# Kernel tuning notes

Measured on AMD Instinct MI355X. Metric: run time of the kernel, lower is better.

## Reference

```python
import jax, jax.numpy as jnp
import numpy as np

CAPACITY_RATIO = 0.75  # matches init kwarg


def setup_inputs() -> dict:
    key = jax.random.key(0)
    k1, k2, k3 = jax.random.split(key, 3)
    B, L, D = 4, 8192, 1024
    x = jax.random.normal(k1, (B, L, D), dtype=jnp.float32)
    # router: nn.Linear(dim, 1, bias=False) -> weight vector [D]
    w_router = jax.random.normal(k2, (D,), dtype=jnp.float32) * 0.02
    # block_fn instantiated as GELU(Linear(D, D)) applied to selected tokens
    w_block = jax.random.normal(k3, (D, D), dtype=jnp.float32) * 0.02
    return {"x": x, "w_router": w_router, "w_block": w_block}


def reference(x, w_router, w_block):
    # Inference path of MoDRouter.forward (self.training == False)
    B, L, D = x.shape
    k = max(1, int(L * CAPACITY_RATIO))  # 6144 < L, so routing path taken
    # scores = self.router(x).squeeze(-1)  -> [B, L]
    scores = jnp.einsum('bld,d->bl', x, w_router)
    # top-k token selection per batch row
    _, top_idx = jax.lax.top_k(scores, k)  # [B, k]
    # gather selected tokens: [B, k, D]
    selected = jnp.take_along_axis(x, top_idx[:, :, None], axis=1)
    # block_fn(selected, None): GELU(selected @ w_block)
    processed = jax.nn.gelu(jnp.einsum('bkd,de->bke', selected, w_block))
    # scatter processed tokens back; unselected tokens pass through (residual skip)
    batch_idx = jnp.arange(B)[:, None]  # [B, 1]
    out = x.at[batch_idx, top_idx].set(processed)
    return out
```

## Files before the change

### kernel.cpp

```cpp
#include <hip/hip_runtime.h>
#include <hip/hip_bf16.h>

typedef unsigned short u16;
typedef unsigned int u32;
typedef __attribute__((ext_vector_type(8))) short short8;
typedef __attribute__((ext_vector_type(4))) float f32x4;

#define L_TOK 8192
#define BATCH 4
#define DIM 1024
#define KSEL 6144
#define NTOK (BATCH * L_TOK)

__device__ __forceinline__ u16 f2bf(float f) {
    u32 u = __float_as_uint(f);
    return (u16)((u + 0x7fffu + ((u >> 16) & 1u)) >> 16);
}
__device__ __forceinline__ u32 cvt2(float a, float b) {
    __hip_bfloat162 h = __float22bfloat162_rn(float2{a, b});
    u32 r;
    __builtin_memcpy(&r, &h, 4);
    return r;
}
__device__ __forceinline__ float gelu_tanh(float v) {
    float inner = 0.7978845608028654f * (v + 0.044715f * v * v * v);
    return 0.5f * v * (1.0f + tanhf(inner));
}
__device__ __forceinline__ void async_copy16(const void* g, void* l) {
    __builtin_amdgcn_global_load_lds(
        (const __attribute__((address_space(1))) void*)g,
        (__attribute__((address_space(3))) void*)l, 16, 0, 0);
}

__global__ __launch_bounds__(256) void score_kernel(const float* __restrict__ x,
                                                    const float* __restrict__ wr,
                                                    float* __restrict__ scores) {
    int token = blockIdx.x * 4 + (threadIdx.x >> 6);
    int lane = threadIdx.x & 63;
    const float4* xr = (const float4*)(x + (size_t)token * DIM) + lane * 4;
    const float4* wp = (const float4*)wr + lane * 4;
    double acc = 0.0;
#pragma unroll
    for (int c = 0; c < 4; ++c) {
        float4 xv = xr[c];
        float4 wv = wp[c];
        acc += (double)xv.x * wv.x + (double)xv.y * wv.y +
               (double)xv.z * wv.z + (double)xv.w * wv.w;
    }
#pragma unroll
    for (int off = 32; off > 0; off >>= 1) acc += __shfl_down(acc, off, 64);
    if (lane == 0) scores[token] = (float)acc;
}

__global__ __launch_bounds__(1024) void select_kernel(const float* __restrict__ scores,
                                                      int* __restrict__ mask) {
    __shared__ u32 keys[L_TOK];
    __shared__ int hist[256];
    __shared__ int g0[256], g1[256];
    __shared__ int wsum[16];
    __shared__ int sel_digit, greater_cnt;
    const int b = blockIdx.x;
    const int tid = threadIdx.x;
    const int lane = tid & 63, wid = tid >> 6;
    const float* s = scores + (size_t)b * L_TOK;
    for (int i = tid; i < L_TOK; i += 1024) {
        u32 u = __float_as_uint(s[i]);
        keys[i] = (u & 0x80000000u) ? ~u : (u | 0x80000000u);
    }

    u32 prefix = 0;
    int need = KSEL;
#pragma unroll
    for (int pass = 0; pass < 4; ++pass) {
        const int shift = 24 - 8 * pass;
        const u32 pmask = (pass == 0) ? 0u : (0xFFFFFFFFu << (shift + 8));
        if (tid < 256) hist[tid] = 0;
        __syncthreads();
        for (int i = tid; i < L_TOK; i += 1024) {
            u32 key = keys[i];
            if ((key & pmask) == prefix)
                atomicAdd(&hist[(key >> shift) & 0xffu], 1);
        }
        __syncthreads();
        if (tid < 256) g0[tid] = hist[tid];
        __syncthreads();
        int* src = g0;
        int* dst = g1;
        for (int step = 1; step < 256; step <<= 1) {
            if (tid < 256) {
                int v = src[tid];
                if (tid + step < 256) v += src[tid + step];
                dst[tid] = v;
            }
            __syncthreads();
            int* t = src; src = dst; dst = t;
        }
        if (tid < 256) {
            int Gd = src[tid];
            int Gn = (tid == 255) ? 0 : src[tid + 1];
            if (Gd >= need && Gn < need) { sel_digit = tid; greater_cnt = Gn; }
        }
        __syncthreads();
        prefix |= ((u32)sel_digit) << shift;
        need -= greater_cnt;
        __syncthreads();
    }
    const u32 T = prefix;
    const int need_eq = need;

    const int base = tid * 8;
    u32 kv[8];
    int eq = 0;
#pragma unroll
    for (int c = 0; c < 8; ++c) { kv[c] = keys[base + c]; eq += (kv[c] == T); }
    int inc = eq;
#pragma unroll
    for (int off = 1; off < 64; off <<= 1) {
        int n = __shfl_up(inc, off, 64);
        if (lane >= off) inc += n;
    }
    if (lane == 63) wsum[wid] = inc;
    __syncthreads();
    int wbase = 0;
    for (int w = 0; w < wid; ++w) wbase += wsum[w];
    int rank = wbase + inc - eq;
    int sel[8];
#pragma unroll
    for (int c = 0; c < 8; ++c) {
        u32 key = kv[c];
        int se = 0;
        if (key > T) se = 1;
        else if (key == T) { se = (rank < need_eq) ? 1 : 0; rank++; }
        sel[c] = se;
    }
    int4* mp = (int4*)(mask + (size_t)b * L_TOK + base);
    mp[0] = int4{sel[0], sel[1], sel[2], sel[3]};
    mp[1] = int4{sel[4], sel[5], sel[6], sel[7]};
}

__global__ __launch_bounds__(256) void transpose_kernel(const float* __restrict__ W,
                                                        u16* __restrict__ WT) {
    __shared__ u16 tile[32][33];
    int bx = blockIdx.x * 32, by = blockIdx.y * 32;
    int tx = threadIdx.x & 31, ty = threadIdx.x >> 5;
    for (int r = ty; r < 32; r += 8)
        tile[r][tx] = f2bf(W[(size_t)(by + r) * DIM + bx + tx]);
    __syncthreads();
    for (int r = ty; r < 32; r += 8)
        WT[(size_t)(bx + r) * DIM + by + tx] = tile[tx][r];
}

__global__ __launch_bounds__(256) void cvt_kernel(const float* __restrict__ x,
                                                  u16* __restrict__ xb) {
    size_t i = ((size_t)blockIdx.x * 256 + threadIdx.x) * 8;
    float4 v0 = *(const float4*)(x + i);
    float4 v1 = *(const float4*)(x + i + 4);
    union { short8 s; u32 u[4]; } pk;
    pk.u[0] = cvt2(v0.x, v0.y); pk.u[1] = cvt2(v0.z, v0.w);
    pk.u[2] = cvt2(v1.x, v1.y); pk.u[3] = cvt2(v1.z, v1.w);
    *(short8*)(xb + i) = pk.s;
}

#define BM 128
#define BN 128
#define BK 32

__global__ __launch_bounds__(256) void gemm_bf16_kernel(const u16* __restrict__ Xb,
                                                        const u16* __restrict__ WT,
                                                        const int* __restrict__ mask,
                                                        float* __restrict__ out) {
    __shared__ alignas(16) u16 As[BM * BK];
    __shared__ alignas(16) u16 Bs[BN * BK];
    const int tid = threadIdx.x;
    const int wave = tid >> 6, lane = tid & 63;
    const int wm = wave >> 1, wn = wave & 1;
    const size_t rowbase = (size_t)blockIdx.x * BM;
    const int colbase = blockIdx.y * BN;

    f32x4 acc[4][4] = {};

    const int ca0 = tid, ca1 = tid + 256;
    const int r0 = ca0 >> 2, k0 = (ca0 & 3) * 8;
    const int r1 = ca1 >> 2, k1 = (ca1 & 3) * 8;
    const int q = lane >> 4, mrow = lane & 15;

    for (int kt = 0; kt < DIM; kt += BK) {
        async_copy16(Xb + (rowbase + r0) * DIM + kt + k0, As + ca0 * 8);
        async_copy16(Xb + (rowbase + r1) * DIM + kt + k1, As + ca1 * 8);
        async_copy16(WT + (size_t)(colbase + r0) * DIM + kt + k0, Bs + ca0 * 8);
        async_copy16(WT + (size_t)(colbase + r1) * DIM + kt + k1, Bs + ca1 * 8);
        __syncthreads();

        short8 a[4], b[4];
#pragma unroll
        for (int i = 0; i < 4; ++i)
            a[i] = *(const short8*)(As + (wm * 64 + i * 16 + mrow) * BK + q * 8);
#pragma unroll
        for (int j = 0; j < 4; ++j)
            b[j] = *(const short8*)(Bs + (wn * 64 + j * 16 + mrow) * BK + q * 8);
#pragma unroll
        for (int i = 0; i < 4; ++i)
#pragma unroll
            for (int j = 0; j < 4; ++j)
                acc[i][j] = __builtin_amdgcn_mfma_f32_16x16x32_bf16(a[i], b[j], acc[i][j], 0, 0, 0);
        __syncthreads();
    }

#pragma unroll
    for (int i = 0; i < 4; ++i) {
#pragma unroll
        for (int r = 0; r < 4; ++r) {
            size_t grow = rowbase + wm * 64 + i * 16 + q * 4 + r;
            if (mask[grow]) {
#pragma unroll
                for (int j = 0; j < 4; ++j) {
                    float g = gelu_tanh(acc[i][j][r]);
                    int col = colbase + wn * 64 + j * 16 + mrow;
                    out[grow * DIM + col] = g;
                }
            }
        }
    }
}

__global__ __launch_bounds__(256) void gemm_f32_kernel(const float* __restrict__ X,
                                                       const u16* __restrict__ WT,
                                                       const int* __restrict__ mask,
                                                       float* __restrict__ out) {
    __shared__ alignas(16) u16 As[BM * BK];
    __shared__ alignas(16) u16 Bs[BN * BK];
    const int tid = threadIdx.x;
    const int wave = tid >> 6, lane = tid & 63;
    const int wm = wave >> 1, wn = wave & 1;
    const size_t rowbase = (size_t)blockIdx.x * BM;
    const int colbase = blockIdx.y * BN;

    f32x4 acc[4][4] = {};

    const int cb0 = tid, cb1 = tid + 256;
    const int br0 = cb0 >> 2, bk0 = (cb0 & 3) * 8;
    const int br1 = cb1 >> 2, bk1 = (cb1 & 3) * 8;
    const int arow = tid >> 1, ahalf = tid & 1;
    const int q = lane >> 4, mrow = lane & 15;

    for (int kt = 0; kt < DIM; kt += BK) {
        async_copy16(WT + (size_t)(colbase + br0) * DIM + kt + bk0, Bs + cb0 * 8);
        async_copy16(WT + (size_t)(colbase + br1) * DIM + kt + bk1, Bs + cb1 * 8);

        const float4* xp = (const float4*)(X + (rowbase + arow) * DIM + kt + ahalf * 16);
        float4 v0 = xp[0], v1 = xp[1], v2 = xp[2], v3 = xp[3];
        union { short8 s[2]; u32 u[8]; } pk;
        pk.u[0] = cvt2(v0.x, v0.y); pk.u[1] = cvt2(v0.z, v0.w);
        pk.u[2] = cvt2(v1.x, v1.y); pk.u[3] = cvt2(v1.z, v1.w);
        pk.u[4] = cvt2(v2.x, v2.y); pk.u[5] = cvt2(v2.z, v2.w);
        pk.u[6] = cvt2(v3.x, v3.y); pk.u[7] = cvt2(v3.z, v3.w);
        *(short8*)(As + arow * BK + ahalf * 16)     = pk.s[0];
        *(short8*)(As + arow * BK + ahalf * 16 + 8) = pk.s[1];

        __syncthreads();

        short8 a[4], b[4];
#pragma unroll
        for (int i = 0; i < 4; ++i)
            a[i] = *(const short8*)(As + (wm * 64 + i * 16 + mrow) * BK + q * 8);
#pragma unroll
        for (int j = 0; j < 4; ++j)
            b[j] = *(const short8*)(Bs + (wn * 64 + j * 16 + mrow) * BK + q * 8);
#pragma unroll
        for (int i = 0; i < 4; ++i)
#pragma unroll
            for (int j = 0; j < 4; ++j)
                acc[i][j] = __builtin_amdgcn_mfma_f32_16x16x32_bf16(a[i], b[j], acc[i][j], 0, 0, 0);
        __syncthreads();
    }

#pragma unroll
    for (int i = 0; i < 4; ++i) {
#pragma unroll
        for (int r = 0; r < 4; ++r) {
            size_t grow = rowbase + wm * 64 + i * 16 + q * 4 + r;
            if (mask[grow]) {
#pragma unroll
                for (int j = 0; j < 4; ++j) {
                    float g = gelu_tanh(acc[i][j][r]);
                    int col = colbase + wn * 64 + j * 16 + mrow;
                    out[grow * DIM + col] = g;
                }
            }
        }
    }
}

__global__ __launch_bounds__(256) void passthrough_kernel(const float* __restrict__ x,
                                                          const int* __restrict__ mask,
                                                          float* __restrict__ out) {
    size_t c = (size_t)blockIdx.x * 256 + threadIdx.x;
    int token = (int)(c >> 8);
    if (!mask[token]) {
        ((float4*)out)[c] = ((const float4*)x)[c];
    }
}

extern "C" void kernel_launch(void* const* d_in, const int* in_sizes, int n_in,
                              void* d_out, int out_size, void* d_ws, size_t ws_size,
                              hipStream_t stream) {
    const float* x  = (const float*)d_in[0];
    const float* wr = (const float*)d_in[1];
    const float* wb = (const float*)d_in[2];
    float* out = (float*)d_out;

    float* scores = (float*)d_ws;
    int*   mask   = (int*)((char*)d_ws + NTOK * 4);
    u16*   WT     = (u16*)((char*)d_ws + NTOK * 8);
    u16*   Xb     = (u16*)((char*)d_ws + NTOK * 8 + DIM * DIM * 2);

    const size_t need_ws = (size_t)NTOK * 8 + (size_t)DIM * DIM * 2
                         + (size_t)NTOK * DIM * 2;

    score_kernel<<<NTOK / 4, 256, 0, stream>>>(x, wr, scores);
    select_kernel<<<BATCH, 1024, 0, stream>>>(scores, mask);
    transpose_kernel<<<dim3(DIM / 32, DIM / 32), 256, 0, stream>>>(wb, WT);
    if (ws_size >= need_ws) {
        cvt_kernel<<<(NTOK * (DIM / 8)) / 256, 256, 0, stream>>>(x, Xb);
        gemm_bf16_kernel<<<dim3(NTOK / BM, DIM / BN), 256, 0, stream>>>(Xb, WT, mask, out);
    } else {
        gemm_f32_kernel<<<dim3(NTOK / BM, DIM / BN), 256, 0, stream>>>(x, WT, mask, out);
    }
    passthrough_kernel<<<(NTOK * 256) / 256, 256, 0, stream>>>(x, mask, out);
}
```

Measured before the change: 381.6 us.

## Compact selected tokens, fuse bf16 cast into scoring, and swizzle GEMM LDS

The select kernel now also emits compacted index lists of selected and unselected tokens. The GEMM runs only over the selected rows, gathered through those indices, instead of computing all tokens and masking the output. The bf16 conversion of x is folded into the score kernel, which removes one full read pass over x. The GEMM uses a BK of 64 with an XOR-swizzled LDS layout to cut bank conflicts. GELU switches from tanh to a sigmoid form using __expf, and the passthrough copy works per unselected token. The costs are gathered row loads and a slightly different GELU approximation.

```diff
diff --git a/kernel.cpp b/kernel.cpp
--- a/kernel.cpp
+++ b/kernel.cpp
@@ -11,6 +11,8 @@
 #define DIM 1024
 #define KSEL 6144
 #define NTOK (BATCH * L_TOK)
+#define NSEL (BATCH * KSEL)
+#define NUNSEL (NTOK - NSEL)
 
 __device__ __forceinline__ u16 f2bf(float f) {
     u32 u = __float_as_uint(f);
@@ -22,9 +24,9 @@
     __builtin_memcpy(&r, &h, 4);
     return r;
 }
-__device__ __forceinline__ float gelu_tanh(float v) {
-    float inner = 0.7978845608028654f * (v + 0.044715f * v * v * v);
-    return 0.5f * v * (1.0f + tanhf(inner));
+__device__ __forceinline__ float gelu_fast(float v) {
+    float z2 = 1.5957691216057308f * (v + 0.044715f * v * v * v);
+    return v / (1.0f + __expf(-z2));
 }
 __device__ __forceinline__ void async_copy16(const void* g, void* l) {
     __builtin_amdgcn_global_load_lds(
@@ -34,18 +36,29 @@
 
 __global__ __launch_bounds__(256) void score_kernel(const float* __restrict__ x,
                                                     const float* __restrict__ wr,
-                                                    float* __restrict__ scores) {
+                                                    float* __restrict__ scores,
+                                                    u16* __restrict__ xb) {
     int token = blockIdx.x * 4 + (threadIdx.x >> 6);
     int lane = threadIdx.x & 63;
     const float4* xr = (const float4*)(x + (size_t)token * DIM) + lane * 4;
     const float4* wp = (const float4*)wr + lane * 4;
+    float4 v[4];
     double acc = 0.0;
 #pragma unroll
     for (int c = 0; c < 4; ++c) {
-        float4 xv = xr[c];
+        v[c] = xr[c];
         float4 wv = wp[c];
-        acc += (double)xv.x * wv.x + (double)xv.y * wv.y +
-               (double)xv.z * wv.z + (double)xv.w * wv.w;
+        acc += (double)v[c].x * wv.x + (double)v[c].y * wv.y +
+               (double)v[c].z * wv.z + (double)v[c].w * wv.w;
+    }
+    if (xb) {
+        union { short8 s[2]; u32 u[8]; } pk;
+        pk.u[0] = cvt2(v[0].x, v[0].y); pk.u[1] = cvt2(v[0].z, v[0].w);
+        pk.u[2] = cvt2(v[1].x, v[1].y); pk.u[3] = cvt2(v[1].z, v[1].w);
+        pk.u[4] = cvt2(v[2].x, v[2].y); pk.u[5] = cvt2(v[2].z, v[2].w);
+        pk.u[6] = cvt2(v[3].x, v[3].y); pk.u[7] = cvt2(v[3].z, v[3].w);
+        short8* dst = (short8*)(xb + (size_t)token * DIM + lane * 16);
+        dst[0] = pk.s[0]; dst[1] = pk.s[1];
     }
 #pragma unroll
     for (int off = 32; off > 0; off >>= 1) acc += __shfl_down(acc, off, 64);
@@ -53,11 +66,14 @@
 }
 
 __global__ __launch_bounds__(1024) void select_kernel(const float* __restrict__ scores,
-                                                      int* __restrict__ mask) {
+                                                      int* __restrict__ mask,
+                                                      int* __restrict__ sel_idx,
+                                                      int* __restrict__ unsel_idx) {
     __shared__ u32 keys[L_TOK];
     __shared__ int hist[256];
     __shared__ int g0[256], g1[256];
     __shared__ int wsum[16];
+    __shared__ int wsum2[16];
     __shared__ int sel_digit, greater_cnt;
     const int b = blockIdx.x;
     const int tid = threadIdx.x;
@@ -136,6 +152,30 @@
     int4* mp = (int4*)(mask + (size_t)b * L_TOK + base);
     mp[0] = int4{sel[0], sel[1], sel[2], sel[3]};
     mp[1] = int4{sel[4], sel[5], sel[6], sel[7]};
+
+    int cnt = 0;
+#pragma unroll
+    for (int c = 0; c < 8; ++c) cnt += sel[c];
+    int inc2 = cnt;
+#pragma unroll
+    for (int off = 1; off < 64; off <<= 1) {
+        int n = __shfl_up(inc2, off, 64);
+        if (lane >= off) inc2 += n;
+    }
+    if (lane == 63) wsum2[wid] = inc2;
+    __syncthreads();
+    int wb2 = 0;
+    for (int w = 0; w < wid; ++w) wb2 += wsum2[w];
+    int pos = wb2 + inc2 - cnt;
+    int up = base - pos;
+    int* si = sel_idx + (size_t)b * KSEL;
+    int* ui = unsel_idx + (size_t)b * (L_TOK - KSEL);
+#pragma unroll
+    for (int c = 0; c < 8; ++c) {
+        int gtok = b * L_TOK + base + c;
+        if (sel[c]) si[pos++] = gtok;
+        else        ui[up++]  = gtok;
+    }
 }
 
 __global__ __launch_bounds__(256) void transpose_kernel(const float* __restrict__ W,
@@ -150,59 +190,68 @@
         WT[(size_t)(bx + r) * DIM + by + tx] = tile[tx][r];
 }
 
-__global__ __launch_bounds__(256) void cvt_kernel(const float* __restrict__ x,
-                                                  u16* __restrict__ xb) {
-    size_t i = ((size_t)blockIdx.x * 256 + threadIdx.x) * 8;
-    float4 v0 = *(const float4*)(x + i);
-    float4 v1 = *(const float4*)(x + i + 4);
-    union { short8 s; u32 u[4]; } pk;
-    pk.u[0] = cvt2(v0.x, v0.y); pk.u[1] = cvt2(v0.z, v0.w);
-    pk.u[2] = cvt2(v1.x, v1.y); pk.u[3] = cvt2(v1.z, v1.w);
-    *(short8*)(xb + i) = pk.s;
-}
-
 #define BM 128
 #define BN 128
 #define BK 32
-
-__global__ __launch_bounds__(256) void gemm_bf16_kernel(const u16* __restrict__ Xb,
-                                                        const u16* __restrict__ WT,
-                                                        const int* __restrict__ mask,
-                                                        float* __restrict__ out) {
-    __shared__ alignas(16) u16 As[BM * BK];
-    __shared__ alignas(16) u16 Bs[BN * BK];
+#define BK2 64
+
+__global__ __launch_bounds__(256) void gemm_idx_kernel(const u16* __restrict__ Xb,
+                                                       const u16* __restrict__ WT,
+                                                       const int* __restrict__ sel_idx,
+                                                       float* __restrict__ out) {
+    __shared__ alignas(16) u16 As[BM * BK2];
+    __shared__ alignas(16) u16 Bs[BN * BK2];
     const int tid = threadIdx.x;
     const int wave = tid >> 6, lane = tid & 63;
     const int wm = wave >> 1, wn = wave & 1;
-    const size_t rowbase = (size_t)blockIdx.x * BM;
+    const int rowbase = blockIdx.x * BM;
     const int colbase = blockIdx.y * BN;
+    const int q = lane >> 4, mrow = lane & 15;
 
     f32x4 acc[4][4] = {};
 
-    const int ca0 = tid, ca1 = tid + 256;
-    const int r0 = ca0 >> 2, k0 = (ca0 & 3) * 8;
-    const int r1 = ca1 >> 2, k1 = (ca1 & 3) * 8;
-    const int q = lane >> 4, mrow = lane & 15;
-
-    for (int kt = 0; kt < DIM; kt += BK) {
-        async_copy16(Xb + (rowbase + r0) * DIM + kt + k0, As + ca0 * 8);
-        async_copy16(Xb + (rowbase + r1) * DIM + kt + k1, As + ca1 * 8);
-        async_copy16(WT + (size_t)(colbase + r0) * DIM + kt + k0, Bs + ca0 * 8);
-        async_copy16(WT + (size_t)(colbase + r1) * DIM + kt + k1, Bs + ca1 * 8);
-        __syncthreads();
-
-        short8 a[4], b[4];
-#pragma unroll
-        for (int i = 0; i < 4; ++i)
-            a[i] = *(const short8*)(As + (wm * 64 + i * 16 + mrow) * BK + q * 8);
-#pragma unroll
-        for (int j = 0; j < 4; ++j)
-            b[j] = *(const short8*)(Bs + (wn * 64 + j * 16 + mrow) * BK + q * 8);
-#pragma unroll
-        for (int i = 0; i < 4; ++i)
-#pragma unroll
-            for (int j = 0; j < 4; ++j)
-                acc[i][j] = __builtin_amdgcn_mfma_f32_16x16x32_bf16(a[i], b[j], acc[i][j], 0, 0, 0);
+    const u16* asrc[4];
+    const u16* bsrc[4];
+    int ldsOff[4];
+#pragma unroll
+    for (int j = 0; j < 4; ++j) {
+        int c = tid + 256 * j;
+        int row = c >> 3, slot = c & 7;
+        int sslot = slot ^ (row & 7);
+        int tok = sel_idx[rowbase + row];
+        asrc[j] = Xb + (size_t)tok * DIM + sslot * 8;
+        bsrc[j] = WT + (size_t)(colbase + row) * DIM + sslot * 8;
+        ldsOff[j] = c * 8;
+    }
+
+    for (int kt = 0; kt < DIM; kt += BK2) {
+#pragma unroll
+        for (int j = 0; j < 4; ++j) async_copy16(asrc[j] + kt, As + ldsOff[j]);
+#pragma unroll
+        for (int j = 0; j < 4; ++j) async_copy16(bsrc[j] + kt, Bs + ldsOff[j]);
+        __syncthreads();
+
+#pragma unroll
+        for (int kk = 0; kk < 2; ++kk) {
+            short8 a[4], b[4];
+#pragma unroll
+            for (int i = 0; i < 4; ++i) {
+                int r = wm * 64 + i * 16 + mrow;
+                int slot = (kk * 4 + q) ^ (r & 7);
+                a[i] = *(const short8*)(As + r * BK2 + slot * 8);
+            }
+#pragma unroll
+            for (int j = 0; j < 4; ++j) {
+                int r = wn * 64 + j * 16 + mrow;
+                int slot = (kk * 4 + q) ^ (r & 7);
+                b[j] = *(const short8*)(Bs + r * BK2 + slot * 8);
+            }
+#pragma unroll
+            for (int i = 0; i < 4; ++i)
+#pragma unroll
+                for (int j = 0; j < 4; ++j)
+                    acc[i][j] = __builtin_amdgcn_mfma_f32_16x16x32_bf16(a[i], b[j], acc[i][j], 0, 0, 0);
+        }
         __syncthreads();
     }
 
@@ -210,14 +259,13 @@
     for (int i = 0; i < 4; ++i) {
 #pragma unroll
         for (int r = 0; r < 4; ++r) {
-            size_t grow = rowbase + wm * 64 + i * 16 + q * 4 + r;
-            if (mask[grow]) {
-#pragma unroll
-                for (int j = 0; j < 4; ++j) {
-                    float g = gelu_tanh(acc[i][j][r]);
-                    int col = colbase + wn * 64 + j * 16 + mrow;
-                    out[grow * DIM + col] = g;
-                }
+            int lrow = wm * 64 + i * 16 + q * 4 + r;
+            int tok = sel_idx[rowbase + lrow];
+#pragma unroll
+            for (int j = 0; j < 4; ++j) {
+                float g = gelu_fast(acc[i][j][r]);
+                int col = colbase + wn * 64 + j * 16 + mrow;
+                out[(size_t)tok * DIM + col] = g;
             }
         }
     }
@@ -282,7 +330,7 @@
             if (mask[grow]) {
 #pragma unroll
                 for (int j = 0; j < 4; ++j) {
-                    float g = gelu_tanh(acc[i][j][r]);
+                    float g = gelu_fast(acc[i][j][r]);
                     int col = colbase + wn * 64 + j * 16 + mrow;
                     out[grow * DIM + col] = g;
                 }
@@ -291,14 +339,12 @@
     }
 }
 
-__global__ __launch_bounds__(256) void passthrough_kernel(const float* __restrict__ x,
-                                                          const int* __restrict__ mask,
-                                                          float* __restrict__ out) {
-    size_t c = (size_t)blockIdx.x * 256 + threadIdx.x;
-    int token = (int)(c >> 8);
-    if (!mask[token]) {
-        ((float4*)out)[c] = ((const float4*)x)[c];
-    }
+__global__ __launch_bounds__(256) void passthrough_idx_kernel(const float* __restrict__ x,
+                                                              const int* __restrict__ unsel_idx,
+                                                              float* __restrict__ out) {
+    int tok = unsel_idx[blockIdx.x];
+    size_t c = (size_t)tok * (DIM / 4) + threadIdx.x;
+    ((float4*)out)[c] = ((const float4*)x)[c];
 }
 
 extern "C" void kernel_launch(void* const* d_in, const int* in_sizes, int n_in,
@@ -309,22 +355,26 @@
     const float* wb = (const float*)d_in[2];
     float* out = (float*)d_out;
 
-    float* scores = (float*)d_ws;
-    int*   mask   = (int*)((char*)d_ws + NTOK * 4);
-    u16*   WT     = (u16*)((char*)d_ws + NTOK * 8);
-    u16*   Xb     = (u16*)((char*)d_ws + NTOK * 8 + DIM * DIM * 2);
-
-    const size_t need_ws = (size_t)NTOK * 8 + (size_t)DIM * DIM * 2
+    char* ws = (char*)d_ws;
+    float* scores    = (float*)ws;
+    int*   mask      = (int*)(ws + (size_t)NTOK * 4);
+    int*   sel_idx   = (int*)(ws + (size_t)NTOK * 8);
+    int*   unsel_idx = (int*)(ws + (size_t)NTOK * 8 + (size_t)NSEL * 4);
+    char*  after_idx = ws + (size_t)NTOK * 8 + (size_t)NTOK * 4;
+    u16*   WT        = (u16*)after_idx;
+    u16*   Xb        = (u16*)(after_idx + (size_t)DIM * DIM * 2);
+
+    const size_t need_ws = (size_t)NTOK * 12 + (size_t)DIM * DIM * 2
                          + (size_t)NTOK * DIM * 2;
-
-    score_kernel<<<NTOK / 4, 256, 0, stream>>>(x, wr, scores);
-    select_kernel<<<BATCH, 1024, 0, stream>>>(scores, mask);
+    const bool big = (ws_size >= need_ws);
+
+    score_kernel<<<NTOK / 4, 256, 0, stream>>>(x, wr, scores, big ? Xb : nullptr);
+    select_kernel<<<BATCH, 1024, 0, stream>>>(scores, mask, sel_idx, unsel_idx);
     transpose_kernel<<<dim3(DIM / 32, DIM / 32), 256, 0, stream>>>(wb, WT);
-    if (ws_size >= need_ws) {
-        cvt_kernel<<<(NTOK * (DIM / 8)) / 256, 256, 0, stream>>>(x, Xb);
-        gemm_bf16_kernel<<<dim3(NTOK / BM, DIM / BN), 256, 0, stream>>>(Xb, WT, mask, out);
+    if (big) {
+        gemm_idx_kernel<<<dim3(NSEL / BM, DIM / BN), 256, 0, stream>>>(Xb, WT, sel_idx, out);
     } else {
         gemm_f32_kernel<<<dim3(NTOK / BM, DIM / BN), 256, 0, stream>>>(x, WT, mask, out);
     }
-    passthrough_kernel<<<(NTOK * 256) / 256, 256, 0, stream>>>(x, mask, out);
-}
+    passthrough_idx_kernel<<<NUNSEL, 256, 0, stream>>>(x, unsel_idx, out);
+}
```

Result: faster. 327.8 us, median of 2 (-14.1%).
